# Kernel optimization log

Measured on AMD Instinct MI355X. Metric: run time of the kernel, lower is better.

The kernel has to match this reference:

```python
import math
import jax, jax.numpy as jnp
import numpy as np

B, L, C, H = 4, 2048, 1024, 16
D = C // H  # head dim = 64

def setup_inputs() -> dict:
    key = jax.random.key(0)
    k1, k2, k3 = jax.random.split(key, 3)
    x = jax.random.normal(k1, (B, L, C), dtype=jnp.float32)
    w_attn = jax.random.normal(k2, (C, 3 * C), dtype=jnp.float32) * (1.0 / math.sqrt(C))
    w_proj = jax.random.normal(k3, (C, C), dtype=jnp.float32) * (1.0 / math.sqrt(C))
    return {"x": x, "w_attn": w_attn, "w_proj": w_proj}

def reference(x, w_attn, w_proj):
    b, l, c = x.shape
    s = x @ w_attn                      # (B,L,3C)
    q, k, v = s[:, :, :c], s[:, :, c:2 * c], s[:, :, 2 * c:]
    # (B,L,H,D) -> (B,H,L,D)
    q = q.reshape(b, l, H, D).transpose(0, 2, 1, 3)
    k = k.reshape(b, l, H, D).transpose(0, 2, 1, 3)
    v = v.reshape(b, l, H, D).transpose(0, 2, 1, 3)
    att = jnp.einsum('bhqd,bhkd->bhqk', q, k) * (1.0 / math.sqrt(D))
    causal = jnp.tril(jnp.ones((l, l), dtype=bool))
    att = jnp.where(causal[None, None], att, -jnp.inf)
    att = jax.nn.softmax(att, axis=-1)
    y = jnp.einsum('bhqk,bhkd->bhqd', att, v)
    y = y.transpose(0, 2, 1, 3).reshape(b, l, c)
    return y @ w_proj
```

## Files before the change

kernel.cpp:

```cpp
#include <hip/hip_runtime.h>
#include <math.h>

typedef unsigned short u16;
typedef unsigned int u32;
typedef __bf16 bf16x8 __attribute__((ext_vector_type(8)));
typedef float f32x4 __attribute__((ext_vector_type(4)));
typedef u16 u16x4 __attribute__((ext_vector_type(4)));
typedef u16 u16x8 __attribute__((ext_vector_type(8)));

#define MFMA16(a, b, c) __builtin_amdgcn_mfma_f32_16x16x32_bf16((a), (b), (c), 0, 0, 0)

#define GLL16(g, l)                                                   \
  __builtin_amdgcn_global_load_lds(                                   \
      (const __attribute__((address_space(1))) void*)(g),             \
      (__attribute__((address_space(3))) void*)(l), 16, 0, 0)

__device__ __forceinline__ u16 f2bf(float f) {
  __bf16 h = (__bf16)f;
  return __builtin_bit_cast(u16, h);
}

__global__ __launch_bounds__(256) void cvt_f32_bf16(const float* __restrict__ in,
                                                    u16* __restrict__ out) {
  size_t i = ((size_t)blockIdx.x * 256 + threadIdx.x) * 4;
  float4 v = *(const float4*)(in + i);
  u16x4 o;
  o[0] = f2bf(v.x); o[1] = f2bf(v.y); o[2] = f2bf(v.z); o[3] = f2bf(v.w);
  *(u16x4*)(out + i) = o;
}

__global__ __launch_bounds__(256) void transpose_w(const float* __restrict__ in,
                                                   u16* __restrict__ out,
                                                   int R, int Cn) {
  __shared__ u16 tile[64][72];
  const int t = threadIdx.x;
  const int tr = blockIdx.y * 64;
  const int tc = blockIdx.x * 64;
#pragma unroll
  for (int p = 0; p < 4; ++p) {
    int chunk = p * 256 + t;
    int r = chunk >> 4, cq = chunk & 15;
    float4 v = *(const float4*)(in + (size_t)(tr + r) * Cn + tc + cq * 4);
    tile[r][cq * 4 + 0] = f2bf(v.x);
    tile[r][cq * 4 + 1] = f2bf(v.y);
    tile[r][cq * 4 + 2] = f2bf(v.z);
    tile[r][cq * 4 + 3] = f2bf(v.w);
  }
  __syncthreads();
#pragma unroll
  for (int p = 0; p < 2; ++p) {
    int chunk = p * 256 + t;
    int c = chunk >> 3, rg = chunk & 7;
    u16x8 v;
#pragma unroll
    for (int i = 0; i < 8; ++i) v[i] = tile[rg * 8 + i][c];
    *(u16x8*)(out + (size_t)(tc + c) * R + tr + rg * 8) = v;
  }
}

__global__ __launch_bounds__(256) void transpose_v(const u16* __restrict__ S,
                                                   u16* __restrict__ VT) {
  __shared__ u16 tile[64][72];
  const int t = threadIdx.x;
  const int lt = blockIdx.x;
  const int bh = blockIdx.y;
  const int b = bh >> 4, h = bh & 15;
  const u16* src = S + ((size_t)b * 2048 + (size_t)lt * 64) * 3072 + 2048 + h * 64;
  u16* dst = VT + (size_t)bh * 64 * 2048 + (size_t)lt * 64;
#pragma unroll
  for (int p = 0; p < 2; ++p) {
    int chunk = p * 256 + t;
    int r = chunk >> 3, cg = chunk & 7;
    u16x8 v = *(const u16x8*)(src + (size_t)r * 3072 + cg * 8);
    *(u16x8*)(&tile[r][cg * 8]) = v;
  }
  __syncthreads();
#pragma unroll
  for (int p = 0; p < 2; ++p) {
    int chunk = p * 256 + t;
    int d = chunk >> 3, rg = chunk & 7;
    u16x8 v;
#pragma unroll
    for (int i = 0; i < 8; ++i) v[i] = tile[rg * 8 + i][d];
    *(u16x8*)(dst + (size_t)d * 2048 + rg * 8) = v;
  }
}

template <bool OUTF32>
__global__ __launch_bounds__(256, 2) void gemm_bt(const u16* __restrict__ A,
                                                  const u16* __restrict__ BT,
                                                  void* __restrict__ Cp,
                                                  int M, int N, int K) {
  __shared__ u16 As[128 * 64];
  __shared__ u16 Bs[128 * 64];
  const int tid = threadIdx.x;
  const int lane = tid & 63;
  const int wid = tid >> 6;
  const int wr = wid >> 1, wc = wid & 1;
  const int rl = lane & 15, kg = lane >> 4;
  const size_t rowA0 = (size_t)blockIdx.y * 128;
  const size_t rowB0 = (size_t)blockIdx.x * 128;

  const int r_st = tid >> 3;
  const int cg_st = tid & 7;

  f32x4 acc[4][4] = {};

  for (int kb = 0; kb < K; kb += 64) {
    __syncthreads();
#pragma unroll
    for (int it = 0; it < 4; ++it) {
      int r = it * 32 + r_st;
      int cgs = cg_st ^ (r & 7);
      GLL16(A + (rowA0 + r) * K + kb + cgs * 8, As + (size_t)r * 64 + cg_st * 8);
      GLL16(BT + (rowB0 + r) * K + kb + cgs * 8, Bs + (size_t)r * 64 + cg_st * 8);
    }
    __syncthreads();

    bf16x8 af[2][4], bfr[2][4];
#pragma unroll
    for (int kk = 0; kk < 2; ++kk) {
      int c8 = kk * 4 + kg;
#pragma unroll
      for (int m = 0; m < 4; ++m) {
        int ra = wr * 64 + m * 16 + rl;
        af[kk][m] = *(const bf16x8*)(As + (size_t)ra * 64 + (size_t)((c8 ^ (ra & 7)) * 8));
        int rb = wc * 64 + m * 16 + rl;
        bfr[kk][m] = *(const bf16x8*)(Bs + (size_t)rb * 64 + (size_t)((c8 ^ (rb & 7)) * 8));
      }
    }
#pragma unroll
    for (int kk = 0; kk < 2; ++kk)
#pragma unroll
      for (int m = 0; m < 4; ++m)
#pragma unroll
        for (int n = 0; n < 4; ++n)
          acc[m][n] = MFMA16(af[kk][m], bfr[kk][n], acc[m][n]);
  }

#pragma unroll
  for (int m = 0; m < 4; ++m)
#pragma unroll
    for (int n = 0; n < 4; ++n)
#pragma unroll
      for (int j = 0; j < 4; ++j) {
        size_t r = rowA0 + wr * 64 + m * 16 + kg * 4 + j;
        size_t c = rowB0 + wc * 64 + n * 16 + rl;
        if constexpr (OUTF32)
          ((float*)Cp)[r * N + c] = acc[m][n][j];
        else
          ((u16*)Cp)[r * N + c] = f2bf(acc[m][n][j]);
      }
}

__global__ __launch_bounds__(256) void attn(const u16* __restrict__ S,
                                            const u16* __restrict__ VT,
                                            u16* __restrict__ Y) {
  __shared__ u16 Ks[2][64 * 64];
  __shared__ u16 Vs[2][64 * 64];
  __shared__ u16 P[4][16][72];
  const int g = blockIdx.x;
  const int t1 = 31 - g;
  const int bh = blockIdx.y;
  const int b = bh >> 4, h = bh & 15;
  const int tid = threadIdx.x, lane = tid & 63, wid = tid >> 6;
  const int rl = lane & 15, kg = lane >> 4;
  const u16* Sq = S + (size_t)b * 2048 * 3072 + h * 64;
  const u16* Sk = Sq + 1024;
  const u16* Vh = VT + (size_t)bh * 64 * 2048;

  const int sr = tid >> 3;
  const int scg = tid & 7;

  const int q0[2] = {g * 64 + wid * 16, t1 * 64 + wid * 16};
  const int tsel[2] = {g, t1};

  bf16x8 qf[2][2];
#pragma unroll
  for (int grp = 0; grp < 2; ++grp)
#pragma unroll
    for (int kc = 0; kc < 2; ++kc)
      qf[grp][kc] = *(const bf16x8*)(Sq + (size_t)(q0[grp] + rl) * 3072 + kc * 32 + kg * 8);

  f32x4 O[2][4] = {};
  float mj[2][4], lj[2][4];
#pragma unroll
  for (int grp = 0; grp < 2; ++grp)
#pragma unroll
    for (int j = 0; j < 4; ++j) { mj[grp][j] = -INFINITY; lj[grp][j] = 0.f; }

  const float SC = 0.125f * 1.44269504088896f;

#define STAGE(buf, kt)                                                          \
  {                                                                             \
    _Pragma("unroll") for (int it = 0; it < 2; ++it) {                          \
      int r = it * 32 + sr;                                                     \
      int cs = scg ^ (r & 7);               \
      GLL16(Sk + (size_t)((kt) * 64 + r) * 3072 + cs * 8,                       \
            &Ks[buf][r * 64 + scg * 8]);                                        \
      GLL16(Vh + (size_t)r * 2048 + (kt) * 64 + cs * 8,                         \
            &Vs[buf][r * 64 + scg * 8]);                                        \
    }                                                                           \
  }

  STAGE(0, 0);
  __syncthreads();

  for (int kt = 0; kt <= t1; ++kt) {
    const int cur = kt & 1;
    if (kt < t1) STAGE(cur ^ 1, kt + 1);

    const u16* Ksb = Ks[cur];
    const u16* Vsb = Vs[cur];

#pragma unroll
    for (int grp = 0; grp < 2; ++grp) {
      if (grp == 0 && kt > g) continue;

      f32x4 sb[4] = {};
#pragma unroll
      for (int nb = 0; nb < 4; ++nb)
#pragma unroll
        for (int kc = 0; kc < 2; ++kc) {
          bf16x8 kf = *(const bf16x8*)(Ksb + (size_t)(nb * 16 + rl) * 64 +
                                       (size_t)(((kc * 4 + kg) ^ (rl & 7)) * 8));
          sb[nb] = MFMA16(qf[grp][kc], kf, sb[nb]);
        }

      const bool diag = (kt == tsel[grp]);
      const int rowq = q0[grp] + kg * 4;
      float sc[4][4];
      float mx4[4] = {mj[grp][0], mj[grp][1], mj[grp][2], mj[grp][3]};
#pragma unroll
      for (int nb = 0; nb < 4; ++nb) {
        int col = kt * 64 + nb * 16 + rl;
#pragma unroll
        for (int j = 0; j < 4; ++j) {
          float v = sb[nb][j] * SC;
          if (diag) v = (col <= rowq + j) ? v : -INFINITY;
          sc[nb][j] = v;
          mx4[j] = fmaxf(mx4[j], v);
        }
      }
#pragma unroll
      for (int off = 1; off < 16; off <<= 1)
#pragma unroll
        for (int j = 0; j < 4; ++j)
          mx4[j] = fmaxf(mx4[j], __shfl_xor(mx4[j], off));

      float scl[4], ps[4];
#pragma unroll
      for (int j = 0; j < 4; ++j) {
        scl[j] = exp2f(mj[grp][j] - mx4[j]);
        mj[grp][j] = mx4[j];
        ps[j] = 0.f;
      }
#pragma unroll
      for (int nb = 0; nb < 4; ++nb)
#pragma unroll
        for (int j = 0; j < 4; ++j) {
          float p = exp2f(sc[nb][j] - mj[grp][j]);
          ps[j] += p;
          P[wid][kg * 4 + j][nb * 16 + rl] = f2bf(p);
        }
#pragma unroll
      for (int off = 1; off < 16; off <<= 1)
#pragma unroll
        for (int j = 0; j < 4; ++j)
          ps[j] += __shfl_xor(ps[j], off);
#pragma unroll
      for (int j = 0; j < 4; ++j) lj[grp][j] = lj[grp][j] * scl[j] + ps[j];
#pragma unroll
      for (int d = 0; d < 4; ++d)
#pragma unroll
        for (int j = 0; j < 4; ++j) O[grp][d][j] *= scl[j];

#pragma unroll
      for (int kc = 0; kc < 2; ++kc) {
        bf16x8 pf = *(const bf16x8*)(&P[wid][rl][kc * 32 + kg * 8]);
#pragma unroll
        for (int d = 0; d < 4; ++d) {
          bf16x8 vf = *(const bf16x8*)(Vsb + (size_t)(d * 16 + rl) * 64 +
                                       (size_t)(((kc * 4 + kg) ^ (rl & 7)) * 8));
          O[grp][d] = MFMA16(pf, vf, O[grp][d]);
        }
      }
    }
    __syncthreads();
  }

#pragma unroll
  for (int grp = 0; grp < 2; ++grp)
#pragma unroll
    for (int j = 0; j < 4; ++j) {
      float inv = 1.0f / lj[grp][j];
#pragma unroll
      for (int d = 0; d < 4; ++d) {
        float val = O[grp][d][j] * inv;
        size_t q = (size_t)b * 2048 + q0[grp] + kg * 4 + j;
        Y[q * 1024 + h * 64 + d * 16 + rl] = f2bf(val);
      }
    }
#undef STAGE
}

extern "C" void kernel_launch(void* const* d_in, const int* in_sizes, int n_in,
                              void* d_out, int out_size, void* d_ws, size_t ws_size,
                              hipStream_t stream) {
  const float* x = (const float*)d_in[0];
  const float* w_attn = (const float*)d_in[1];
  const float* w_proj = (const float*)d_in[2];
  float* out = (float*)d_out;

  u16* S = (u16*)d_ws;
  u16* WT1 = S + (size_t)8192 * 3072;
  u16* WT2 = WT1 + (size_t)3072 * 1024;
  u16* VT = WT2 + (size_t)1024 * 1024;
  u16* Y = VT + (size_t)64 * 64 * 2048;
  u16* XB = Y + (size_t)8192 * 1024;

  cvt_f32_bf16<<<8192, 256, 0, stream>>>(x, XB);
  transpose_w<<<dim3(3072 / 64, 1024 / 64), 256, 0, stream>>>(w_attn, WT1, 1024, 3072);
  transpose_w<<<dim3(1024 / 64, 1024 / 64), 256, 0, stream>>>(w_proj, WT2, 1024, 1024);
  gemm_bt<false><<<dim3(3072 / 128, 8192 / 128), 256, 0, stream>>>(XB, WT1, S, 8192, 3072, 1024);
  transpose_v<<<dim3(32, 64), 256, 0, stream>>>(S, VT);
  attn<<<dim3(16, 64), 256, 0, stream>>>(S, VT, Y);
  gemm_bt<true><<<dim3(1024 / 128, 8192 / 128), 256, 0, stream>>>(Y, WT2, out, 8192, 1024, 1024);
}
```

Before: 342.3 us.

## Rewrite attention inner loop with 32x32 MFMA and register-resident P

The attention kernel switches from 16x16x32 MFMA tiles to 32x32x16 tiles and computes S transposed (K as A operand), so each lane owns one query row. Softmax reductions become in-register with a single cross-half shuffle, P is repacked to bf16 through lane shuffles instead of a shared-memory round trip, and Q is pre-scaled once. The two query groups are now split across wave pairs rather than looped per wave, so waves of the light group sit idle after their diagonal tile, which can cost load balance. It also adds s_setprio around the MFMA sections and vectorized output stores.

```diff
diff --git a/kernel.cpp b/kernel.cpp
--- a/kernel.cpp
+++ b/kernel.cpp
@@ -5,10 +5,13 @@
 typedef unsigned int u32;
 typedef __bf16 bf16x8 __attribute__((ext_vector_type(8)));
 typedef float f32x4 __attribute__((ext_vector_type(4)));
+typedef float f32x16 __attribute__((ext_vector_type(16)));
 typedef u16 u16x4 __attribute__((ext_vector_type(4)));
 typedef u16 u16x8 __attribute__((ext_vector_type(8)));
+typedef u32 u32x4 __attribute__((ext_vector_type(4)));
 
 #define MFMA16(a, b, c) __builtin_amdgcn_mfma_f32_16x16x32_bf16((a), (b), (c), 0, 0, 0)
+#define MFMA32(a, b, c) __builtin_amdgcn_mfma_f32_32x32x16_bf16((a), (b), (c), 0, 0, 0)
 
 #define GLL16(g, l)                                                   \
   __builtin_amdgcn_global_load_lds(                                   \
@@ -18,6 +21,9 @@
 __device__ __forceinline__ u16 f2bf(float f) {
   __bf16 h = (__bf16)f;
   return __builtin_bit_cast(u16, h);
+}
+__device__ __forceinline__ u32 pack2(float a, float b) {
+  return (u32)f2bf(a) | ((u32)f2bf(b) << 16);
 }
 
 __global__ __launch_bounds__(256) void cvt_f32_bf16(const float* __restrict__ in,
@@ -158,38 +164,23 @@
                                             u16* __restrict__ Y) {
   __shared__ u16 Ks[2][64 * 64];
   __shared__ u16 Vs[2][64 * 64];
-  __shared__ u16 P[4][16][72];
   const int g = blockIdx.x;
   const int t1 = 31 - g;
   const int bh = blockIdx.y;
   const int b = bh >> 4, h = bh & 15;
   const int tid = threadIdx.x, lane = tid & 63, wid = tid >> 6;
-  const int rl = lane & 15, kg = lane >> 4;
+  const int ql = lane & 31;
+  const int hi = lane >> 5;
+  const int grp = wid >> 1;
+  const int hw = wid & 1;
+  const int myt = grp ? t1 : g;
+  const int qrow = myt * 64 + hw * 32 + ql;
+
   const u16* Sq = S + (size_t)b * 2048 * 3072 + h * 64;
   const u16* Sk = Sq + 1024;
   const u16* Vh = VT + (size_t)bh * 64 * 2048;
 
-  const int sr = tid >> 3;
-  const int scg = tid & 7;
-
-  const int q0[2] = {g * 64 + wid * 16, t1 * 64 + wid * 16};
-  const int tsel[2] = {g, t1};
-
-  bf16x8 qf[2][2];
-#pragma unroll
-  for (int grp = 0; grp < 2; ++grp)
-#pragma unroll
-    for (int kc = 0; kc < 2; ++kc)
-      qf[grp][kc] = *(const bf16x8*)(Sq + (size_t)(q0[grp] + rl) * 3072 + kc * 32 + kg * 8);
-
-  f32x4 O[2][4] = {};
-  float mj[2][4], lj[2][4];
-#pragma unroll
-  for (int grp = 0; grp < 2; ++grp)
-#pragma unroll
-    for (int j = 0; j < 4; ++j) { mj[grp][j] = -INFINITY; lj[grp][j] = 0.f; }
-
-  const float SC = 0.125f * 1.44269504088896f;
+  const int sr = tid >> 3, scg = tid & 7;
 
 #define STAGE(buf, kt)                                                          \
   {                                                                             \
@@ -203,103 +194,131 @@
     }                                                                           \
   }
 
+  const float SC = 0.125f * 1.44269504088896f;
+  bf16x8 qf[4];
+#pragma unroll
+  for (int s4 = 0; s4 < 4; ++s4) {
+    bf16x8 q = *(const bf16x8*)(Sq + (size_t)qrow * 3072 + s4 * 16 + hi * 8);
+    bf16x8 qs;
+#pragma unroll
+    for (int i = 0; i < 8; ++i) qs[i] = (__bf16)((float)q[i] * SC);
+    qf[s4] = qs;
+  }
+
+  f32x16 O0 = {}, O1 = {};
+  float mj = -INFINITY, lj = 0.f;
+
   STAGE(0, 0);
   __syncthreads();
 
   for (int kt = 0; kt <= t1; ++kt) {
     const int cur = kt & 1;
     if (kt < t1) STAGE(cur ^ 1, kt + 1);
-
     const u16* Ksb = Ks[cur];
     const u16* Vsb = Vs[cur];
 
-#pragma unroll
-    for (int grp = 0; grp < 2; ++grp) {
-      if (grp == 0 && kt > g) continue;
-
-      f32x4 sb[4] = {};
-#pragma unroll
-      for (int nb = 0; nb < 4; ++nb)
-#pragma unroll
-        for (int kc = 0; kc < 2; ++kc) {
-          bf16x8 kf = *(const bf16x8*)(Ksb + (size_t)(nb * 16 + rl) * 64 +
-                                       (size_t)(((kc * 4 + kg) ^ (rl & 7)) * 8));
-          sb[nb] = MFMA16(qf[grp][kc], kf, sb[nb]);
+    const bool active = (grp == 1) || (kt <= g);
+    if (active) {
+      f32x16 s0 = {}, s1 = {};
+      __builtin_amdgcn_s_setprio(1);
+#pragma unroll
+      for (int s4 = 0; s4 < 4; ++s4) {
+        int cix = (2 * s4 + hi) ^ (ql & 7);
+        bf16x8 kf0 = *(const bf16x8*)(Ksb + (size_t)ql * 64 + cix * 8);
+        bf16x8 kf1 = *(const bf16x8*)(Ksb + (size_t)(32 + ql) * 64 + cix * 8);
+        s0 = MFMA32(kf0, qf[s4], s0);
+        s1 = MFMA32(kf1, qf[s4], s1);
+      }
+      __builtin_amdgcn_s_setprio(0);
+
+      if (kt == myt) {
+        const int lim = hw * 32 + ql;
+#pragma unroll
+        for (int r = 0; r < 16; ++r) {
+          int c0 = (r & 3) + 8 * (r >> 2) + 4 * hi;
+          s0[r] = (c0 <= lim) ? s0[r] : -INFINITY;
+          s1[r] = (32 + c0 <= lim) ? s1[r] : -INFINITY;
         }
-
-      const bool diag = (kt == tsel[grp]);
-      const int rowq = q0[grp] + kg * 4;
-      float sc[4][4];
-      float mx4[4] = {mj[grp][0], mj[grp][1], mj[grp][2], mj[grp][3]};
-#pragma unroll
-      for (int nb = 0; nb < 4; ++nb) {
-        int col = kt * 64 + nb * 16 + rl;
-#pragma unroll
-        for (int j = 0; j < 4; ++j) {
-          float v = sb[nb][j] * SC;
-          if (diag) v = (col <= rowq + j) ? v : -INFINITY;
-          sc[nb][j] = v;
-          mx4[j] = fmaxf(mx4[j], v);
-        }
-      }
-#pragma unroll
-      for (int off = 1; off < 16; off <<= 1)
-#pragma unroll
-        for (int j = 0; j < 4; ++j)
-          mx4[j] = fmaxf(mx4[j], __shfl_xor(mx4[j], off));
-
-      float scl[4], ps[4];
-#pragma unroll
-      for (int j = 0; j < 4; ++j) {
-        scl[j] = exp2f(mj[grp][j] - mx4[j]);
-        mj[grp][j] = mx4[j];
-        ps[j] = 0.f;
-      }
-#pragma unroll
-      for (int nb = 0; nb < 4; ++nb)
-#pragma unroll
-        for (int j = 0; j < 4; ++j) {
-          float p = exp2f(sc[nb][j] - mj[grp][j]);
-          ps[j] += p;
-          P[wid][kg * 4 + j][nb * 16 + rl] = f2bf(p);
-        }
-#pragma unroll
-      for (int off = 1; off < 16; off <<= 1)
-#pragma unroll
-        for (int j = 0; j < 4; ++j)
-          ps[j] += __shfl_xor(ps[j], off);
-#pragma unroll
-      for (int j = 0; j < 4; ++j) lj[grp][j] = lj[grp][j] * scl[j] + ps[j];
-#pragma unroll
-      for (int d = 0; d < 4; ++d)
-#pragma unroll
-        for (int j = 0; j < 4; ++j) O[grp][d][j] *= scl[j];
-
-#pragma unroll
-      for (int kc = 0; kc < 2; ++kc) {
-        bf16x8 pf = *(const bf16x8*)(&P[wid][rl][kc * 32 + kg * 8]);
-#pragma unroll
-        for (int d = 0; d < 4; ++d) {
-          bf16x8 vf = *(const bf16x8*)(Vsb + (size_t)(d * 16 + rl) * 64 +
-                                       (size_t)(((kc * 4 + kg) ^ (rl & 7)) * 8));
-          O[grp][d] = MFMA16(pf, vf, O[grp][d]);
-        }
-      }
+      }
+
+      float t16[16];
+#pragma unroll
+      for (int r = 0; r < 16; ++r) t16[r] = fmaxf(s0[r], s1[r]);
+#pragma unroll
+      for (int off = 8; off >= 1; off >>= 1)
+#pragma unroll
+        for (int i = 0; i < 8; ++i)
+          if (i < off) t16[i] = fmaxf(t16[i], t16[i + off]);
+      float rmax = fmaxf(t16[0], __shfl_xor(t16[0], 32));
+      float mn = fmaxf(mj, rmax);
+      float scl = exp2f(mj - mn);
+      mj = mn;
+#pragma unroll
+      for (int r = 0; r < 16; ++r) {
+        s0[r] = exp2f(s0[r] - mn);
+        s1[r] = exp2f(s1[r] - mn);
+      }
+      float a16[16];
+#pragma unroll
+      for (int r = 0; r < 16; ++r) a16[r] = s0[r] + s1[r];
+#pragma unroll
+      for (int off = 8; off >= 1; off >>= 1)
+#pragma unroll
+        for (int i = 0; i < 8; ++i)
+          if (i < off) a16[i] += a16[i + off];
+      float rsum = a16[0] + __shfl_xor(a16[0], 32);
+      lj = lj * scl + rsum;
+#pragma unroll
+      for (int r = 0; r < 16; ++r) { O0[r] *= scl; O1[r] *= scl; }
+
+      __builtin_amdgcn_s_setprio(1);
+#pragma unroll
+      for (int Sstep = 0; Sstep < 4; ++Sstep) {
+        const int kb = Sstep >> 1, s = Sstep & 1;
+        float e0 = kb ? s1[8 * s + 0] : s0[8 * s + 0];
+        float e1 = kb ? s1[8 * s + 1] : s0[8 * s + 1];
+        float e2 = kb ? s1[8 * s + 2] : s0[8 * s + 2];
+        float e3 = kb ? s1[8 * s + 3] : s0[8 * s + 3];
+        float f0 = kb ? s1[8 * s + 4] : s0[8 * s + 4];
+        float f1 = kb ? s1[8 * s + 5] : s0[8 * s + 5];
+        float f2 = kb ? s1[8 * s + 6] : s0[8 * s + 6];
+        float f3 = kb ? s1[8 * s + 7] : s0[8 * s + 7];
+        u32 a0 = pack2(e0, e1), a1 = pack2(e2, e3);
+        u32 b0 = pack2(f0, f1), b1 = pack2(f2, f3);
+        u32 s0w = hi ? a0 : b0;
+        u32 s1w = hi ? a1 : b1;
+        u32 r0 = (u32)__shfl_xor((int)s0w, 32);
+        u32 r1 = (u32)__shfl_xor((int)s1w, 32);
+        u32x4 pw;
+        pw[0] = hi ? r0 : a0;
+        pw[1] = hi ? r1 : a1;
+        pw[2] = hi ? b0 : r0;
+        pw[3] = hi ? b1 : r1;
+        bf16x8 pf = __builtin_bit_cast(bf16x8, pw);
+        int cix = (2 * Sstep + hi) ^ (ql & 7);
+        bf16x8 vf0 = *(const bf16x8*)(Vsb + (size_t)ql * 64 + cix * 8);
+        bf16x8 vf1 = *(const bf16x8*)(Vsb + (size_t)(32 + ql) * 64 + cix * 8);
+        O0 = MFMA32(vf0, pf, O0);
+        O1 = MFMA32(vf1, pf, O1);
+      }
+      __builtin_amdgcn_s_setprio(0);
     }
     __syncthreads();
   }
 
-#pragma unroll
-  for (int grp = 0; grp < 2; ++grp)
-#pragma unroll
-    for (int j = 0; j < 4; ++j) {
-      float inv = 1.0f / lj[grp][j];
-#pragma unroll
-      for (int d = 0; d < 4; ++d) {
-        float val = O[grp][d][j] * inv;
-        size_t q = (size_t)b * 2048 + q0[grp] + kg * 4 + j;
-        Y[q * 1024 + h * 64 + d * 16 + rl] = f2bf(val);
-      }
+  const float inv = 1.0f / lj;
+  u16* yrow = Y + (size_t)(b * 2048 + qrow) * 1024 + h * 64;
+#pragma unroll
+  for (int db = 0; db < 2; ++db)
+#pragma unroll
+    for (int rq = 0; rq < 4; ++rq) {
+      u16x4 o;
+#pragma unroll
+      for (int j = 0; j < 4; ++j) {
+        float v = (db ? O1[rq * 4 + j] : O0[rq * 4 + j]) * inv;
+        o[j] = f2bf(v);
+      }
+      *(u16x4*)(yrow + db * 32 + 8 * rq + 4 * hi) = o;
     }
 #undef STAGE
 }
```

After: 343.5 us. Within noise of the previous version (+0.3%).
